# Kernel tuning notes

Measured on AMD Instinct MI355X. Metric: run time of the kernel, lower is better.

The kernel has to match this reference:

```python
import jax, jax.numpy as jnp
import numpy as np

B, HIDDEN, NH, MAX_S = 8, 4096, 32, 4096
HD = HIDDEN // NH  # 128
POS = 2047  # current cache write position (tokens 0..POS-1 already cached)


def setup_inputs() -> dict:
    key = jax.random.key(0)
    ks = jax.random.split(key, 7)
    x = jax.random.normal(ks[0], (B, 1, HIDDEN), dtype=jnp.float32)
    cached_k = jax.random.normal(ks[1], (B, NH, MAX_S, HD), dtype=jnp.float32)
    cached_v = jax.random.normal(ks[2], (B, NH, MAX_S, HD), dtype=jnp.float32)
    scale = 0.02
    wq = jax.random.normal(ks[3], (HIDDEN, HIDDEN), dtype=jnp.float32) * scale
    wk = jax.random.normal(ks[4], (HIDDEN, HIDDEN), dtype=jnp.float32) * scale
    wv = jax.random.normal(ks[5], (HIDDEN, HIDDEN), dtype=jnp.float32) * scale
    wo = jax.random.normal(ks[6], (HIDDEN, HIDDEN), dtype=jnp.float32) * scale
    return {"x": x, "cached_k": cached_k, "cached_v": cached_v,
            "wq": wq, "wk": wk, "wv": wv, "wo": wo, "cached_pos": POS}


def reference(x, cached_k, cached_v, wq, wk, wv, wo, cached_pos):
    # Decode step: seq_len == 1 (is_training=False path of the torch module).
    b, s, hidden = x.shape  # s == 1
    # Projections (torch Linear: y = x @ W.T), reshape to [B, H, 1, D]
    q = (x @ wq.T).reshape(b, s, NH, HD).transpose(0, 2, 1, 3)
    k = (x @ wk.T).reshape(b, s, NH, HD).transpose(0, 2, 1, 3)
    v = (x @ wv.T).reshape(b, s, NH, HD).transpose(0, 2, 1, 3)
    # Append new token's K/V into the cache at cached_pos (static python int)
    ck = cached_k.at[:, :, cached_pos, :].set(k[:, :, 0, :])
    cv = cached_v.at[:, :, cached_pos, :].set(v[:, :, 0, :])
    # Attend over the valid prefix [0, cached_pos]
    kk = ck[:, :, :cached_pos + 1, :]  # [B, H, T, D]
    vv = cv[:, :, :cached_pos + 1, :]
    scores = jnp.einsum('bhqd,bhkd->bhqk', q, kk) / jnp.sqrt(jnp.float32(HD))
    att = jax.nn.softmax(scores, axis=-1)  # stable softmax == module's _softmax
    out = jnp.einsum('bhqk,bhkd->bhqd', att, vv)  # [B, H, 1, D]
    out = out.transpose(0, 2, 1, 3).reshape(b, s, hidden)
    return out @ wo.T
```

## Files before the change

kernel.cpp:

```cpp
#include <hip/hip_runtime.h>
#include <cmath>

#define B_     8
#define NH_    32
#define HD_    128
#define HID_   4096
#define MAXS_  4096
#define NPAIR_ (B_ * NH_)
#define NSPLIT_ 4
#define PSTR_  132
#define NEG_BIG_ (-1e30f)

typedef float f4_ __attribute__((ext_vector_type(4)));

__device__ __forceinline__ f4_ ntload4(const float* p) {
  return __builtin_nontemporal_load((const f4_*)p);
}
__device__ __forceinline__ f4_ ld4(const float* p) {
  return *(const f4_*)p;
}
__device__ __forceinline__ float dot4(f4_ a, f4_ b) {
  f4_ m = a * b;
  return m.x + m.y + m.z + m.w;
}

__global__ __launch_bounds__(256) void gemv_rows(
    const float* __restrict__ W0, const float* __restrict__ W1,
    const float* __restrict__ W2, const float* __restrict__ x,
    float* __restrict__ out)
{
  const int bid = blockIdx.x;
  const int m   = bid >> 9;
  const int rb  = (bid & 511) << 3;
  const float* __restrict__ W = (m == 0) ? W0 : ((m == 1) ? W1 : W2);
  float* o = out + m * (B_ * HID_);

  const int wib  = threadIdx.x >> 6;
  const int lane = threadIdx.x & 63;
  const int r0   = rb + wib * 2;

  float acc[2][8];
#pragma unroll
  for (int r = 0; r < 2; ++r)
#pragma unroll
    for (int b = 0; b < 8; ++b) acc[r][b] = 0.f;

  const float* Wp = W + (size_t)r0 * HID_ + lane * 4;
#pragma unroll 2
  for (int u = 0; u < 16; ++u) {
    const int j = u * 256;
    f4_ w0 = ld4(Wp + j);
    f4_ w1 = ld4(Wp + j + HID_);
#pragma unroll
    for (int b = 0; b < 8; ++b) {
      f4_ xb = ld4(x + b * HID_ + j + lane * 4);
      acc[0][b] += dot4(w0, xb);
      acc[1][b] += dot4(w1, xb);
    }
  }

#pragma unroll
  for (int r = 0; r < 2; ++r)
#pragma unroll
    for (int b = 0; b < 8; ++b) {
      float v = acc[r][b];
#pragma unroll
      for (int off = 32; off; off >>= 1) v += __shfl_xor(v, off);
      acc[r][b] = v;
    }

  if (lane == 0) {
#pragma unroll
    for (int r = 0; r < 2; ++r)
#pragma unroll
      for (int b = 0; b < 8; ++b)
        o[(size_t)b * HID_ + r0 + r] = acc[r][b];
  }
}

__global__ __launch_bounds__(256, 4) void attn_partial(
    const float* __restrict__ qkv, const float* __restrict__ ck,
    const float* __restrict__ cv, const int* __restrict__ ppos,
    float* __restrict__ part)
{
  __shared__ float sm[4], sl[4];
  __shared__ float sacc[4][HD_];

  const int pos  = *ppos;
  const int bid  = blockIdx.x;
  const int pair = bid >> 2;
  const int s    = bid & (NSPLIT_ - 1);
  const int b    = pair >> 5;
  const int h    = pair & (NH_ - 1);
  const int w    = threadIdx.x >> 6;
  const int lane = threadIdx.x & 63;
  const int half = lane >> 5, l32 = lane & 31;
  const int k0   = s * 512 + w * 128;

  float m = NEG_BIG_, l = 0.f;
  f4_ acc = (f4_)0.f;

  if (k0 <= pos) {
    const float scale = 0.08838834764831845f;
    f4_ q4 = ld4(qkv + b * HID_ + h * HD_ + l32 * 4) * scale;
    const float* kfresh = qkv + B_ * HID_     + b * HID_ + h * HD_;
    const float* vfresh = qkv + 2 * B_ * HID_ + b * HID_ + h * HD_;
    const float* ckh = ck + ((size_t)(b * NH_ + h)) * MAXS_ * HD_;
    const float* cvh = cv + ((size_t)(b * NH_ + h)) * MAXS_ * HD_;

    for (int c = 0; c < 8; ++c) {
      const int kbase = k0 + c * 16;
      f4_ k4[8], v4[8];
#pragma unroll
      for (int j = 0; j < 8; ++j) {
        const int ki = kbase + 2 * j + half;
        const float* kp = (ki == pos) ? kfresh : (ckh + (size_t)ki * HD_);
        const float* vp = (ki == pos) ? vfresh : (cvh + (size_t)ki * HD_);
        k4[j] = ntload4(kp + l32 * 4);
        v4[j] = ntload4(vp + l32 * 4);
      }

      float sc[8];
#pragma unroll
      for (int j = 0; j < 8; ++j) sc[j] = dot4(q4, k4[j]);

#pragma unroll
      for (int off = 16; off >= 1; off >>= 1)
#pragma unroll
        for (int j = 0; j < 8; ++j) sc[j] += __shfl_xor(sc[j], off);

#pragma unroll
      for (int j = 0; j < 8; ++j) {
        const int ki = kbase + 2 * j + half;
        if (ki > pos) sc[j] = -INFINITY;
      }

      const float cm = fmaxf(fmaxf(fmaxf(sc[0], sc[1]), fmaxf(sc[2], sc[3])),
                             fmaxf(fmaxf(sc[4], sc[5]), fmaxf(sc[6], sc[7])));
      const float mn   = fmaxf(m, cm);
      const float corr = __expf(m - mn);
      float p[8], ps = 0.f;
#pragma unroll
      for (int j = 0; j < 8; ++j) { p[j] = __expf(sc[j] - mn); ps += p[j]; }
      l = l * corr + ps;
      acc *= corr;
#pragma unroll
      for (int j = 0; j < 8; ++j) acc += p[j] * v4[j];
      m = mn;
    }
  }

  const float mo = __shfl_xor(m, 32);
  const float lo = __shfl_xor(l, 32);
  f4_ ao;
  ao.x = __shfl_xor(acc.x, 32); ao.y = __shfl_xor(acc.y, 32);
  ao.z = __shfl_xor(acc.z, 32); ao.w = __shfl_xor(acc.w, 32);
  const float mm = fmaxf(m, mo);
  const float w0 = __expf(m - mm), w1 = __expf(mo - mm);
  const float lm = l * w0 + lo * w1;
  f4_ am = acc * w0 + ao * w1;

  if (half == 0) {
    *(f4_*)&sacc[w][l32 * 4] = am;
    if (l32 == 0) { sm[w] = mm; sl[w] = lm; }
  }
  __syncthreads();

  if (threadIdx.x < 32) {
    const int t = threadIdx.x;
    float mg = NEG_BIG_;
#pragma unroll
    for (int u = 0; u < 4; ++u)
      if (sl[u] > 0.f) mg = fmaxf(mg, sm[u]);
    float ls = 0.f;
    f4_ o = (f4_)0.f;
#pragma unroll
    for (int u = 0; u < 4; ++u)
      if (sl[u] > 0.f) {
        const float wu = __expf(sm[u] - mg);
        ls += sl[u] * wu;
        o  += wu * ld4(&sacc[u][t * 4]);
      }
    float* pb = part + (size_t)bid * PSTR_;
    *(f4_*)(pb + 4 + t * 4) = o;
    if (t == 0) { pb[0] = (ls > 0.f) ? mg : NEG_BIG_; pb[1] = ls; }
  }
}

__global__ __launch_bounds__(128) void attn_combine(
    const float* __restrict__ part, float* __restrict__ attnout)
{
  const int pair = blockIdx.x;
  const int d    = threadIdx.x;
  const float* pb = part + (size_t)pair * NSPLIT_ * PSTR_;

  float mg = NEG_BIG_;
#pragma unroll
  for (int u = 0; u < NSPLIT_; ++u) {
    const float lu = pb[u * PSTR_ + 1];
    if (lu > 0.f) mg = fmaxf(mg, pb[u * PSTR_]);
  }
  float ls = 0.f, o = 0.f;
#pragma unroll
  for (int u = 0; u < NSPLIT_; ++u) {
    const float lu = pb[u * PSTR_ + 1];
    if (lu > 0.f) {
      const float wu = __expf(pb[u * PSTR_] - mg);
      ls += lu * wu;
      o  += wu * pb[u * PSTR_ + 4 + d];
    }
  }
  attnout[pair * HD_ + d] = o / ls;
}

extern "C" void kernel_launch(void* const* d_in, const int* in_sizes, int n_in,
                              void* d_out, int out_size, void* d_ws, size_t ws_size,
                              hipStream_t stream) {
  const float* x  = (const float*)d_in[0];
  const float* ck = (const float*)d_in[1];
  const float* cv = (const float*)d_in[2];
  const float* wq = (const float*)d_in[3];
  const float* wk = (const float*)d_in[4];
  const float* wv = (const float*)d_in[5];
  const float* wo = (const float*)d_in[6];
  const int* pos  = (const int*)d_in[7];
  float* out = (float*)d_out;
  float* ws  = (float*)d_ws;

  float* qkv     = ws;
  float* part    = ws + 3 * B_ * HID_;
  float* attnout = part + NPAIR_ * NSPLIT_ * PSTR_;

  gemv_rows<<<3 * 512, 256, 0, stream>>>(wq, wk, wv, x, qkv);
  attn_partial<<<NPAIR_ * NSPLIT_, 256, 0, stream>>>(qkv, ck, cv, pos, part);
  attn_combine<<<NPAIR_, 128, 0, stream>>>(part, attnout);
  gemv_rows<<<512, 256, 0, stream>>>(wo, wo, wo, attnout, out);
}
```

Baseline: 198.1 us.

## Stage GEMV weight rows into LDS with double-buffered async global_load_lds

Replaces the register-load GEMV with a version that copies weight rows into shared memory using the direct global-to-LDS load builtin, double-buffered so the next 256-column slab loads while the current one is consumed. The QKV projection also processes 16 rows per block (4 per wave) with half as many blocks, which amortises the activation loads over more rows. The goal is to keep more weight bytes in flight on this memory-bound step. In exchange it adds a block-wide barrier every iteration, uses 16–32 KB of LDS per block, and halves the number of blocks for the QKV GEMV.

```diff
diff --git a/kernel.cpp b/kernel.cpp
--- a/kernel.cpp
+++ b/kernel.cpp
@@ -1,5 +1,6 @@
 #include <hip/hip_runtime.h>
 #include <cmath>
+#include <cstdint>
 
 #define B_     8
 #define NH_    32
@@ -24,43 +25,75 @@
   return m.x + m.y + m.z + m.w;
 }
 
-__global__ __launch_bounds__(256) void gemv_rows(
+__device__ __forceinline__ void stage_row16(const float* gsrc, unsigned ldsoff) {
+  __builtin_amdgcn_global_load_lds(
+      (__attribute__((address_space(1))) void*)(uintptr_t)gsrc,
+      (__attribute__((address_space(3))) void*)ldsoff,
+      16, 0, 0);
+}
+
+template<int TR>
+__global__ __launch_bounds__(256) void gemv_lds(
     const float* __restrict__ W0, const float* __restrict__ W1,
     const float* __restrict__ W2, const float* __restrict__ x,
-    float* __restrict__ out)
+    float* __restrict__ out, int nb_per_mat)
 {
+  extern __shared__ float dyn[];
+  constexpr int RW = TR / 4;
+
   const int bid = blockIdx.x;
-  const int m   = bid >> 9;
-  const int rb  = (bid & 511) << 3;
+  const int m   = bid / nb_per_mat;
+  const int rb  = (bid % nb_per_mat) * TR;
   const float* __restrict__ W = (m == 0) ? W0 : ((m == 1) ? W1 : W2);
   float* o = out + m * (B_ * HID_);
 
   const int wib  = threadIdx.x >> 6;
   const int lane = threadIdx.x & 63;
-  const int r0   = rb + wib * 2;
-
-  float acc[2][8];
-#pragma unroll
-  for (int r = 0; r < 2; ++r)
+  const int r0   = rb + wib * RW;
+
+  float acc[RW][8];
+#pragma unroll
+  for (int r = 0; r < RW; ++r)
 #pragma unroll
     for (int b = 0; b < 8; ++b) acc[r][b] = 0.f;
 
-  const float* Wp = W + (size_t)r0 * HID_ + lane * 4;
-#pragma unroll 2
+#define STAGE_(buf, u)                                                        \
+  {                                                                           \
+    _Pragma("unroll")                                                         \
+    for (int rr = 0; rr < RW; ++rr) {                                         \
+      const int row = wib * RW + rr;                                          \
+      stage_row16(W + (size_t)(rb + row) * HID_ + (u) * 256 + lane * 4,       \
+                  (unsigned)(((buf) * TR + row) * 1024));                     \
+    }                                                                         \
+  }
+
+  STAGE_(0, 0);
+  __syncthreads();
+
+  int cur = 0;
   for (int u = 0; u < 16; ++u) {
+    if (u + 1 < 16) STAGE_(cur ^ 1, u + 1);
+
     const int j = u * 256;
-    f4_ w0 = ld4(Wp + j);
-    f4_ w1 = ld4(Wp + j + HID_);
-#pragma unroll
-    for (int b = 0; b < 8; ++b) {
-      f4_ xb = ld4(x + b * HID_ + j + lane * 4);
-      acc[0][b] += dot4(w0, xb);
-      acc[1][b] += dot4(w1, xb);
-    }
-  }
-
-#pragma unroll
-  for (int r = 0; r < 2; ++r)
+    f4_ xv[8];
+#pragma unroll
+    for (int b = 0; b < 8; ++b) xv[b] = ld4(x + b * HID_ + j + lane * 4);
+    f4_ wv[RW];
+#pragma unroll
+    for (int rr = 0; rr < RW; ++rr)
+      wv[rr] = ld4(&dyn[(cur * TR + wib * RW + rr) * 256 + lane * 4]);
+#pragma unroll
+    for (int rr = 0; rr < RW; ++rr)
+#pragma unroll
+      for (int b = 0; b < 8; ++b) acc[rr][b] += dot4(wv[rr], xv[b]);
+
+    __syncthreads();
+    cur ^= 1;
+  }
+#undef STAGE_
+
+#pragma unroll
+  for (int r = 0; r < RW; ++r)
 #pragma unroll
     for (int b = 0; b < 8; ++b) {
       float v = acc[r][b];
@@ -71,7 +104,7 @@
 
   if (lane == 0) {
 #pragma unroll
-    for (int r = 0; r < 2; ++r)
+    for (int r = 0; r < RW; ++r)
 #pragma unroll
       for (int b = 0; b < 8; ++b)
         o[(size_t)b * HID_ + r0 + r] = acc[r][b];
@@ -231,8 +264,8 @@
   float* part    = ws + 3 * B_ * HID_;
   float* attnout = part + NPAIR_ * NSPLIT_ * PSTR_;
 
-  gemv_rows<<<3 * 512, 256, 0, stream>>>(wq, wk, wv, x, qkv);
+  gemv_lds<16><<<3 * 256, 256, 32768, stream>>>(wq, wk, wv, x, qkv, 256);
   attn_partial<<<NPAIR_ * NSPLIT_, 256, 0, stream>>>(qkv, ck, cv, pos, part);
   attn_combine<<<NPAIR_, 128, 0, stream>>>(part, attnout);
-  gemv_rows<<<512, 256, 0, stream>>>(wo, wo, wo, attnout, out);
-}
+  gemv_lds<8><<<512, 256, 16384, stream>>>(wo, wo, wo, attnout, out, 512);
+}
```

Result: slower. 235.5 us (+18.9%).

## Rework GEMV to one wave per eight rows with double-buffered weight loads

Applied to the files above, without the earlier changes.

The projection GEMV now uses single-wave blocks, each computing 8 output rows for all 8 batch rows. Every x load is reused across 8 weight rows instead of 2, which cuts redundant activation traffic. Weight loads are double-buffered in registers so the next chunk is fetched while the current one is accumulated. The 64-entry accumulator array plus 16 weight vectors raise register pressure and may lower occupancy, and blocks are now 64 threads, giving fewer resident waves per CU to hide memory latency.

```diff
diff --git a/kernel.cpp b/kernel.cpp
--- a/kernel.cpp
+++ b/kernel.cpp
@@ -24,43 +24,66 @@
   return m.x + m.y + m.z + m.w;
 }
 
-__global__ __launch_bounds__(256) void gemv_rows(
+__global__ __launch_bounds__(64) void gemv8(
     const float* __restrict__ W0, const float* __restrict__ W1,
     const float* __restrict__ W2, const float* __restrict__ x,
-    float* __restrict__ out)
+    float* __restrict__ out, int nb_per_mat)
 {
   const int bid = blockIdx.x;
-  const int m   = bid >> 9;
-  const int rb  = (bid & 511) << 3;
+  const int m   = bid / nb_per_mat;
+  const int r0  = (bid % nb_per_mat) * 8;
   const float* __restrict__ W = (m == 0) ? W0 : ((m == 1) ? W1 : W2);
   float* o = out + m * (B_ * HID_);
 
-  const int wib  = threadIdx.x >> 6;
-  const int lane = threadIdx.x & 63;
-  const int r0   = rb + wib * 2;
-
-  float acc[2][8];
-#pragma unroll
-  for (int r = 0; r < 2; ++r)
+  const int lane = threadIdx.x;
+
+  float acc[8][8];
+#pragma unroll
+  for (int r = 0; r < 8; ++r)
 #pragma unroll
     for (int b = 0; b < 8; ++b) acc[r][b] = 0.f;
 
   const float* Wp = W + (size_t)r0 * HID_ + lane * 4;
-#pragma unroll 2
-  for (int u = 0; u < 16; ++u) {
-    const int j = u * 256;
-    f4_ w0 = ld4(Wp + j);
-    f4_ w1 = ld4(Wp + j + HID_);
-#pragma unroll
-    for (int b = 0; b < 8; ++b) {
-      f4_ xb = ld4(x + b * HID_ + j + lane * 4);
-      acc[0][b] += dot4(w0, xb);
-      acc[1][b] += dot4(w1, xb);
-    }
-  }
-
-#pragma unroll
-  for (int r = 0; r < 2; ++r)
+  const float* xp = x + lane * 4;
+
+  f4_ wa[8], wb[8];
+#pragma unroll
+  for (int r = 0; r < 8; ++r) wa[r] = ld4(Wp + (size_t)r * HID_);
+
+#pragma unroll 1
+  for (int u = 0; u < 16; u += 2) {
+    {
+      const int j = u * 256;
+      f4_ xv[8];
+#pragma unroll
+      for (int b = 0; b < 8; ++b) xv[b] = ld4(xp + b * HID_ + j);
+#pragma unroll
+      for (int r = 0; r < 8; ++r)
+        wb[r] = ld4(Wp + (size_t)r * HID_ + j + 256);
+#pragma unroll
+      for (int r = 0; r < 8; ++r)
+#pragma unroll
+        for (int b = 0; b < 8; ++b) acc[r][b] += dot4(wa[r], xv[b]);
+    }
+    {
+      const int j = (u + 1) * 256;
+      f4_ xv[8];
+#pragma unroll
+      for (int b = 0; b < 8; ++b) xv[b] = ld4(xp + b * HID_ + j);
+      if (u + 2 < 16) {
+#pragma unroll
+        for (int r = 0; r < 8; ++r)
+          wa[r] = ld4(Wp + (size_t)r * HID_ + j + 256);
+      }
+#pragma unroll
+      for (int r = 0; r < 8; ++r)
+#pragma unroll
+        for (int b = 0; b < 8; ++b) acc[r][b] += dot4(wb[r], xv[b]);
+    }
+  }
+
+#pragma unroll
+  for (int r = 0; r < 8; ++r)
 #pragma unroll
     for (int b = 0; b < 8; ++b) {
       float v = acc[r][b];
@@ -71,7 +94,7 @@
 
   if (lane == 0) {
 #pragma unroll
-    for (int r = 0; r < 2; ++r)
+    for (int r = 0; r < 8; ++r)
 #pragma unroll
       for (int b = 0; b < 8; ++b)
         o[(size_t)b * HID_ + r0 + r] = acc[r][b];
@@ -231,8 +254,8 @@
   float* part    = ws + 3 * B_ * HID_;
   float* attnout = part + NPAIR_ * NSPLIT_ * PSTR_;
 
-  gemv_rows<<<3 * 512, 256, 0, stream>>>(wq, wk, wv, x, qkv);
+  gemv8<<<3 * 512, 64, 0, stream>>>(wq, wk, wv, x, qkv, 512);
   attn_partial<<<NPAIR_ * NSPLIT_, 256, 0, stream>>>(qkv, ck, cv, pos, part);
   attn_combine<<<NPAIR_, 128, 0, stream>>>(part, attnout);
-  gemv_rows<<<512, 256, 0, stream>>>(wo, wo, wo, attnout, out);
-}
+  gemv8<<<512, 64, 0, stream>>>(wo, wo, wo, attnout, out, 512);
+}
```

Result: faster. 178.5 us (-9.9%).
